# Performance work log

Measured on AMD Instinct MI355X. Metric: run time of the kernel, lower is better.

The kernel has to match this reference:

```python
import jax, jax.numpy as jnp
import numpy as np

B, IN, H = 4096, 1024, 2048


def setup_inputs() -> dict:
    key = jax.random.key(0)
    k1, k2, k3, k4 = jax.random.split(key, 4)
    x = jax.random.normal(k1, (B, IN), dtype=jnp.float32)
    h_prev = jax.random.normal(k2, (B, H), dtype=jnp.float32)
    c_prev = jax.random.normal(k3, (B, H), dtype=jnp.float32)
    # Fused weight for the 5 gate Linears (Wf, Wi, Wc, Wo, We), columns stacked.
    # Scaled like PyTorch Linear default init (~uniform(-1/sqrt(fan_in))).
    W = jax.random.normal(k4, (IN + H, 5 * H), dtype=jnp.float32) / jnp.sqrt(jnp.float32(IN + H))
    b = jnp.zeros((5 * H,), dtype=jnp.float32)
    return {"x": x, "h_prev": h_prev, "c_prev": c_prev, "W": W, "b": b}


def reference(x, h_prev, c_prev, W, b):
    combined = jnp.concatenate([x, h_prev], axis=1)          # [B, IN+H]
    z = combined @ W + b                                      # [B, 5H] single fused GEMM
    f, i, c_hat, o, e = jnp.split(z, 5, axis=1)
    ft = jax.nn.sigmoid(f)
    it = jax.nn.sigmoid(i)
    ct_hat = jnp.tanh(c_hat)
    ot = jax.nn.sigmoid(o)
    et = jax.nn.sigmoid(e)
    ct = ft * c_prev + it * ct_hat
    ht = ot * jnp.tanh(ct)
    ht = et * jnp.exp(ht) + (1.0 - et) * ht
    return ht, ct
```

## Files before the change

kernel.cpp:

```cpp
#include <hip/hip_runtime.h>
#include <hip/hip_bf16.h>
#include <stdint.h>

#define B_  4096
#define IN_ 1024
#define H_  2048
#define K_  (IN_ + H_)
#define N_  (5 * H_)

#define BM 128
#define BN 128
#define BK 32

typedef __attribute__((ext_vector_type(8))) short   short8;
typedef __attribute__((ext_vector_type(4))) float   f32x4;

__device__ __forceinline__ unsigned short f2bf(float f) {
  union { float f; unsigned u; } cv; cv.f = f;
  unsigned u = cv.u;
  u += 0x7fffu + ((u >> 16) & 1u);
  return (unsigned short)(u >> 16);
}

__device__ __forceinline__ float bf2f(unsigned short s) {
  union { unsigned u; float f; } cv; cv.u = ((unsigned)s) << 16;
  return cv.f;
}

__device__ __forceinline__ void async16(const unsigned short* g, unsigned short* l) {
  __builtin_amdgcn_global_load_lds(
      (const __attribute__((address_space(1))) unsigned int*)g,
      (__attribute__((address_space(3))) unsigned int*)(void*)l,
      16, 0, 0);
}

__global__ void build_combined(const float* __restrict__ x,
                               const float* __restrict__ h,
                               unsigned short* __restrict__ out) {
  const int row = blockIdx.x;
  const float4* xr = (const float4*)(x + (size_t)row * IN_);
  const float4* hr = (const float4*)(h + (size_t)row * H_);
  uint2* orow = (uint2*)(out + (size_t)row * K_);
  for (int c = threadIdx.x; c < K_ / 4; c += 256) {
    float4 v = (c < IN_ / 4) ? xr[c] : hr[c - IN_ / 4];
    uint2 p;
    p.x = (unsigned)f2bf(v.x) | ((unsigned)f2bf(v.y) << 16);
    p.y = (unsigned)f2bf(v.z) | ((unsigned)f2bf(v.w) << 16);
    orow[c] = p;
  }
}

__global__ void transpose_convert(const float* __restrict__ W,
                                  unsigned short* __restrict__ Wt) {
  __shared__ float tile[64][33];
  const int n0 = blockIdx.x * 32;
  const int k0 = blockIdx.y * 64;
  const int tx = threadIdx.x;
  const int ty = threadIdx.y;
  #pragma unroll
  for (int kk = ty; kk < 64; kk += 8)
    tile[kk][tx] = W[(size_t)(k0 + kk) * N_ + n0 + tx];
  __syncthreads();
  #pragma unroll
  for (int nn = ty; nn < 32; nn += 8) {
    unsigned lo = f2bf(tile[2 * tx][nn]);
    unsigned hi = f2bf(tile[2 * tx + 1][nn]);
    *(unsigned*)(&Wt[(size_t)(n0 + nn) * K_ + k0 + 2 * tx]) = lo | (hi << 16);
  }
}

__global__ __launch_bounds__(256) void gemm_z(
    const unsigned short* __restrict__ A,
    const unsigned short* __restrict__ Bt,
    unsigned short* __restrict__ Z)
{
  __shared__ unsigned short As[BM * BK];
  __shared__ unsigned short Bs[BN * BK];

  const int tid  = threadIdx.x;
  const int wave = tid >> 6;
  const int lane = tid & 63;
  const int quad = lane >> 4;
  const int lr   = lane & 15;

  const int ntiles = N_ / BN;
  const int tile_n = blockIdx.x % ntiles;
  const int tile_m = blockIdx.x / ntiles;

  const int wm = (wave >> 1) * 64;
  const int wn = (wave & 1) * 64;

  f32x4 acc[4][4];
  #pragma unroll
  for (int i = 0; i < 4; ++i)
    #pragma unroll
    for (int j = 0; j < 4; ++j)
      acc[i][j] = (f32x4){0.f, 0.f, 0.f, 0.f};

  const int srow = wave * 32 + (lane >> 2);
  const int scol = (lane & 3) * 8;
  const unsigned short* aP = A  + ((size_t)tile_m * BM + srow) * K_ + scol;
  const unsigned short* bP = Bt + ((size_t)tile_n * BN + srow) * K_ + scol;
  unsigned short* aL0 = &As[(wave * 32)      * BK];
  unsigned short* aL1 = &As[(wave * 32 + 16) * BK];
  unsigned short* bL0 = &Bs[(wave * 32)      * BK];
  unsigned short* bL1 = &Bs[(wave * 32 + 16) * BK];
  const size_t k16 = (size_t)16 * K_;

  for (int k0 = 0; k0 < K_; k0 += BK) {
    async16(aP + k0,       aL0);
    async16(aP + k0 + k16, aL1);
    async16(bP + k0,       bL0);
    async16(bP + k0 + k16, bL1);
    __syncthreads();

    short8 af[4], bf[4];
    #pragma unroll
    for (int mi = 0; mi < 4; ++mi)
      af[mi] = *(const short8*)&As[(wm + mi * 16 + lr) * BK + quad * 8];
    #pragma unroll
    for (int ni = 0; ni < 4; ++ni)
      bf[ni] = *(const short8*)&Bs[(wn + ni * 16 + lr) * BK + quad * 8];

    #pragma unroll
    for (int mi = 0; mi < 4; ++mi)
      #pragma unroll
      for (int ni = 0; ni < 4; ++ni)
        acc[mi][ni] = __builtin_amdgcn_mfma_f32_16x16x32_bf16(
            af[mi], bf[ni], acc[mi][ni], 0, 0, 0);

    __syncthreads();
  }

  const size_t colbase = (size_t)tile_n * BN + wn + lr;
  #pragma unroll
  for (int mi = 0; mi < 4; ++mi) {
    #pragma unroll
    for (int r = 0; r < 4; ++r) {
      const size_t row = (size_t)tile_m * BM + wm + mi * 16 + quad * 4 + r;
      unsigned short* zp = Z + row * N_ + colbase;
      #pragma unroll
      for (int ni = 0; ni < 4; ++ni)
        zp[ni * 16] = f2bf(acc[mi][ni][r]);
    }
  }
}

__global__ void epilogue(const unsigned short* __restrict__ Z,
                         const float* __restrict__ c_prev,
                         const float* __restrict__ b,
                         float* __restrict__ out) {
  const int idx = blockIdx.x * blockDim.x + threadIdx.x;
  const int r = idx >> 11;
  const int j = idx & (H_ - 1);
  const unsigned short* zr = Z + (size_t)r * N_ + j;

  const float zf = bf2f(zr[0])        + b[j];
  const float zi = bf2f(zr[H_])       + b[j + H_];
  const float zc = bf2f(zr[2 * H_])   + b[j + 2 * H_];
  const float zo = bf2f(zr[3 * H_])   + b[j + 3 * H_];
  const float ze = bf2f(zr[4 * H_])   + b[j + 4 * H_];

  const float ft = 1.f / (1.f + __expf(-zf));
  const float it = 1.f / (1.f + __expf(-zi));
  const float ch = tanhf(zc);
  const float ot = 1.f / (1.f + __expf(-zo));
  const float et = 1.f / (1.f + __expf(-ze));

  const float ct = ft * c_prev[idx] + it * ch;
  const float th = tanhf(ct);
  float ht = ot * th;
  ht = et * __expf(ht) + (1.f - et) * ht;

  out[idx] = ht;
  out[(size_t)B_ * H_ + idx] = ct;
}

extern "C" void kernel_launch(void* const* d_in, const int* in_sizes, int n_in,
                              void* d_out, int out_size, void* d_ws, size_t ws_size,
                              hipStream_t stream) {
  const float* x = (const float*)d_in[0];
  const float* h = (const float*)d_in[1];
  const float* c = (const float*)d_in[2];
  const float* W = (const float*)d_in[3];
  const float* b = (const float*)d_in[4];
  float* out = (float*)d_out;

  char* ws = (char*)d_ws;
  unsigned short* combined = (unsigned short*)ws;
  unsigned short* Wt = (unsigned short*)(ws + (size_t)25165824);
  unsigned short* Z  = (unsigned short*)(ws + (size_t)25165824 + 62914560);

  build_combined<<<B_, 256, 0, stream>>>(x, h, combined);
  transpose_convert<<<dim3(N_ / 32, K_ / 64), dim3(32, 8), 0, stream>>>(W, Wt);
  gemm_z<<<(B_ / BM) * (N_ / BN), 256, 0, stream>>>(combined, Wt, Z);
  epilogue<<<(B_ * H_) / 256, 256, 0, stream>>>(Z, c, b, out);
}
```

Baseline: 608.4 us.

## Swizzle GEMM LDS layout, vectorize transpose and epilogue, use fast math

The GEMM's global-to-LDS loads and fragment reads now use an XOR swizzle on the k-chunk slot, meant to remove LDS bank conflicts. The weight transpose handles 64x64 tiles with float4 loads and 16-byte bf16 stores. The epilogue processes two columns per thread with vectorized loads and stores. Its sigmoid and tanh now use a reciprocal intrinsic and an exp-based tanh. The fast tanh trades some accuracy near saturation and could overflow for large inputs.

Measured after the change: 583.5 us. 4.1% less time.

```diff
diff --git a/kernel.cpp b/kernel.cpp
--- a/kernel.cpp
+++ b/kernel.cpp
@@ -14,6 +14,7 @@
 
 typedef __attribute__((ext_vector_type(8))) short   short8;
 typedef __attribute__((ext_vector_type(4))) float   f32x4;
+typedef __attribute__((ext_vector_type(8))) unsigned short ushort8;
 
 __device__ __forceinline__ unsigned short f2bf(float f) {
   union { float f; unsigned u; } cv; cv.f = f;
@@ -32,6 +33,13 @@
       (const __attribute__((address_space(1))) unsigned int*)g,
       (__attribute__((address_space(3))) unsigned int*)(void*)l,
       16, 0, 0);
+}
+
+__device__ __forceinline__ float fsig(float x) {
+  return __builtin_amdgcn_rcpf(1.f + __expf(-x));
+}
+__device__ __forceinline__ float ftanh(float x) {
+  return 1.f - 2.f * __builtin_amdgcn_rcpf(__expf(2.f * x) + 1.f);
 }
 
 __global__ void build_combined(const float* __restrict__ x,
@@ -50,22 +58,32 @@
   }
 }
 
-__global__ void transpose_convert(const float* __restrict__ W,
-                                  unsigned short* __restrict__ Wt) {
-  __shared__ float tile[64][33];
-  const int n0 = blockIdx.x * 32;
+__global__ __launch_bounds__(256) void transpose_convert(
+    const float* __restrict__ W, unsigned short* __restrict__ Wt) {
+  __shared__ float tile[64][65];
+  const int n0 = blockIdx.x * 64;
   const int k0 = blockIdx.y * 64;
-  const int tx = threadIdx.x;
-  const int ty = threadIdx.y;
-  #pragma unroll
-  for (int kk = ty; kk < 64; kk += 8)
-    tile[kk][tx] = W[(size_t)(k0 + kk) * N_ + n0 + tx];
+  const int t  = threadIdx.x;
+
+  const int lrow = t >> 2;
+  #pragma unroll
+  for (int i = 0; i < 4; ++i) {
+    const int col4 = i * 4 + (t & 3);
+    const float4 v = *(const float4*)&W[(size_t)(k0 + lrow) * N_ + n0 + col4 * 4];
+    float* dst = &tile[lrow][col4 * 4];
+    dst[0] = v.x; dst[1] = v.y; dst[2] = v.z; dst[3] = v.w;
+  }
   __syncthreads();
-  #pragma unroll
-  for (int nn = ty; nn < 32; nn += 8) {
-    unsigned lo = f2bf(tile[2 * tx][nn]);
-    unsigned hi = f2bf(tile[2 * tx + 1][nn]);
-    *(unsigned*)(&Wt[(size_t)(n0 + nn) * K_ + k0 + 2 * tx]) = lo | (hi << 16);
+
+  #pragma unroll
+  for (int i = 0; i < 2; ++i) {
+    const int c2 = t + i * 256;
+    const int nn = c2 >> 3;
+    const int kc = (c2 & 7) * 8;
+    ushort8 p;
+    #pragma unroll
+    for (int u = 0; u < 8; ++u) p[u] = f2bf(tile[kc + u][nn]);
+    *(ushort8*)&Wt[(size_t)(n0 + nn) * K_ + k0 + kc] = p;
   }
 }
 
@@ -98,7 +116,7 @@
       acc[i][j] = (f32x4){0.f, 0.f, 0.f, 0.f};
 
   const int srow = wave * 32 + (lane >> 2);
-  const int scol = (lane & 3) * 8;
+  const int scol = (((lane & 3) ^ ((lane >> 3) & 3))) * 8;
   const unsigned short* aP = A  + ((size_t)tile_m * BM + srow) * K_ + scol;
   const unsigned short* bP = Bt + ((size_t)tile_n * BN + srow) * K_ + scol;
   unsigned short* aL0 = &As[(wave * 32)      * BK];
@@ -107,6 +125,8 @@
   unsigned short* bL1 = &Bs[(wave * 32 + 16) * BK];
   const size_t k16 = (size_t)16 * K_;
 
+  const int rslot = (quad ^ ((lr >> 1) & 3)) * 8;
+
   for (int k0 = 0; k0 < K_; k0 += BK) {
     async16(aP + k0,       aL0);
     async16(aP + k0 + k16, aL1);
@@ -117,10 +137,10 @@
     short8 af[4], bf[4];
     #pragma unroll
     for (int mi = 0; mi < 4; ++mi)
-      af[mi] = *(const short8*)&As[(wm + mi * 16 + lr) * BK + quad * 8];
+      af[mi] = *(const short8*)&As[(wm + mi * 16 + lr) * BK + rslot];
     #pragma unroll
     for (int ni = 0; ni < 4; ++ni)
-      bf[ni] = *(const short8*)&Bs[(wn + ni * 16 + lr) * BK + quad * 8];
+      bf[ni] = *(const short8*)&Bs[(wn + ni * 16 + lr) * BK + rslot];
 
     #pragma unroll
     for (int mi = 0; mi < 4; ++mi)
@@ -146,34 +166,52 @@
   }
 }
 
-__global__ void epilogue(const unsigned short* __restrict__ Z,
-                         const float* __restrict__ c_prev,
-                         const float* __restrict__ b,
-                         float* __restrict__ out) {
-  const int idx = blockIdx.x * blockDim.x + threadIdx.x;
-  const int r = idx >> 11;
-  const int j = idx & (H_ - 1);
+__global__ __launch_bounds__(256) void epilogue(
+    const unsigned short* __restrict__ Z,
+    const float* __restrict__ c_prev,
+    const float* __restrict__ b,
+    float* __restrict__ out) {
+  const int idx2 = blockIdx.x * 256 + threadIdx.x;
+  const int r  = idx2 >> 10;
+  const int j  = (idx2 & 1023) * 2;
   const unsigned short* zr = Z + (size_t)r * N_ + j;
 
-  const float zf = bf2f(zr[0])        + b[j];
-  const float zi = bf2f(zr[H_])       + b[j + H_];
-  const float zc = bf2f(zr[2 * H_])   + b[j + 2 * H_];
-  const float zo = bf2f(zr[3 * H_])   + b[j + 3 * H_];
-  const float ze = bf2f(zr[4 * H_])   + b[j + 4 * H_];
-
-  const float ft = 1.f / (1.f + __expf(-zf));
-  const float it = 1.f / (1.f + __expf(-zi));
-  const float ch = tanhf(zc);
-  const float ot = 1.f / (1.f + __expf(-zo));
-  const float et = 1.f / (1.f + __expf(-ze));
-
-  const float ct = ft * c_prev[idx] + it * ch;
-  const float th = tanhf(ct);
-  float ht = ot * th;
-  ht = et * __expf(ht) + (1.f - et) * ht;
-
-  out[idx] = ht;
-  out[(size_t)B_ * H_ + idx] = ct;
+  unsigned zg[5];
+  float2 bg[5];
+  #pragma unroll
+  for (int g = 0; g < 5; ++g) {
+    zg[g] = *(const unsigned*)(zr + g * H_);
+    bg[g] = *(const float2*)(b + g * H_ + j);
+  }
+  const float2 cp = *(const float2*)(c_prev + (size_t)r * H_ + j);
+
+  float ht[2], ct[2];
+  #pragma unroll
+  for (int u = 0; u < 2; ++u) {
+    const float zf = bf2f((unsigned short)(zg[0] >> (16 * u))) + (u ? bg[0].y : bg[0].x);
+    const float zi = bf2f((unsigned short)(zg[1] >> (16 * u))) + (u ? bg[1].y : bg[1].x);
+    const float zc = bf2f((unsigned short)(zg[2] >> (16 * u))) + (u ? bg[2].y : bg[2].x);
+    const float zo = bf2f((unsigned short)(zg[3] >> (16 * u))) + (u ? bg[3].y : bg[3].x);
+    const float ze = bf2f((unsigned short)(zg[4] >> (16 * u))) + (u ? bg[4].y : bg[4].x);
+
+    const float ft = fsig(zf);
+    const float it = fsig(zi);
+    const float ch = ftanh(zc);
+    const float ot = fsig(zo);
+    const float et = fsig(ze);
+
+    const float c0 = u ? cp.y : cp.x;
+    const float cn = ft * c0 + it * ch;
+    const float th = ftanh(cn);
+    float hn = ot * th;
+    hn = et * __expf(hn) + (1.f - et) * hn;
+    ht[u] = hn; ct[u] = cn;
+  }
+
+  float2* o1 = (float2*)(out + (size_t)r * H_ + j);
+  float2* o2 = (float2*)(out + (size_t)B_ * H_ + (size_t)r * H_ + j);
+  *o1 = make_float2(ht[0], ht[1]);
+  *o2 = make_float2(ct[0], ct[1]);
 }
 
 extern "C" void kernel_launch(void* const* d_in, const int* in_sizes, int n_in,
@@ -192,7 +230,7 @@
   unsigned short* Z  = (unsigned short*)(ws + (size_t)25165824 + 62914560);
 
   build_combined<<<B_, 256, 0, stream>>>(x, h, combined);
-  transpose_convert<<<dim3(N_ / 32, K_ / 64), dim3(32, 8), 0, stream>>>(W, Wt);
+  transpose_convert<<<dim3(N_ / 64, K_ / 64), 256, 0, stream>>>(W, Wt);
   gemm_z<<<(B_ / BM) * (N_ / BN), 256, 0, stream>>>(combined, Wt, Z);
-  epilogue<<<(B_ * H_) / 256, 256, 0, stream>>>(Z, c, b, out);
-}
+  epilogue<<<(B_ * H_) / 2 / 256, 256, 0, stream>>>(Z, c, b, out);
+}
```
